# Kernel optimization log

Hardware: AMD Instinct MI355X
Metric: run time of the kernel (lower is better)

The kernel has to match this reference:

```python
import jax, jax.numpy as jnp
import numpy as np
from jax import lax

HEATMAP_THRESH = 0.1


def _conv(x, w, b, stride=1):
    y = lax.conv_general_dilated(x, w, (stride, stride), 'SAME',
                                 dimension_numbers=('NCHW', 'OIHW', 'NCHW'))
    return y + b[None, :, None, None]


def _maxpool2(x):
    return lax.reduce_window(x, -jnp.inf, lax.max, (1, 1, 2, 2), (1, 1, 2, 2), 'VALID')


def _up2(x):
    return jnp.repeat(jnp.repeat(x, 2, axis=2), 2, axis=3)


def _find_peaks_mask(hm, thresh):
    # Vectorized equivalent of the CPU nested-loop _find_peaks:
    # interior pixel is a peak iff v > thresh and v >= its 4 axial neighbors.
    c = hm[:, :, 1:-1, 1:-1]
    m = ((c > thresh)
         & (c >= hm[:, :, :-2, 1:-1]) & (c >= hm[:, :, 2:, 1:-1])
         & (c >= hm[:, :, 1:-1, :-2]) & (c >= hm[:, :, 1:-1, 2:]))
    return jnp.pad(m, ((0, 0), (0, 0), (1, 1), (1, 1)))  # border never a peak


def _param(key, shape):
    fan_in = int(np.prod(shape[1:]))
    return jax.random.normal(key, shape, jnp.float32) / np.sqrt(fan_in)


_SHAPES = {
    'w_d1': (32, 3, 3, 3), 'w_d2': (64, 32, 3, 3), 'w_bn': (128, 64, 3, 3),
    'w_u1': (64, 192, 3, 3), 'w_u2': (32, 96, 3, 3), 'w_seg': (1, 32, 1, 1),
    'w_p1': (64, 4, 3, 3), 'w_p2': (128, 64, 3, 3),
    'w_hm': (17, 128, 1, 1), 'w_paf': (32, 128, 1, 1),
}


def setup_inputs() -> dict:
    key = jax.random.key(0)
    ks = jax.random.split(key, 1 + len(_SHAPES))
    B, H, W = 8, 384, 384
    inp = {'x': jax.random.normal(ks[0], (B, 3, H, W), jnp.float32)}
    for i, (n, s) in enumerate(_SHAPES.items()):
        inp[n] = _param(ks[i + 1], s)
        inp[n.replace('w_', 'b_')] = jnp.zeros((s[0],), jnp.float32)
    return inp


def _forward(x, w_d1, b_d1, w_d2, b_d2, w_bn, b_bn, w_u1, b_u1, w_u2, b_u2,
             w_seg, b_seg, w_p1, b_p1, w_p2, b_p2, w_hm, b_hm, w_paf, b_paf):
    # --- UNet segmentation ---
    d1 = jax.nn.relu(_conv(x, w_d1, b_d1))                    # [B,32,384,384]
    d2 = jax.nn.relu(_conv(_maxpool2(d1), w_d2, b_d2))        # [B,64,192,192]
    bn = jax.nn.relu(_conv(_maxpool2(d2), w_bn, b_bn))        # [B,128,96,96]
    u1 = jax.nn.relu(_conv(jnp.concatenate([_up2(bn), d2], 1), w_u1, b_u1))  # [B,64,192,192]
    u2 = jax.nn.relu(_conv(jnp.concatenate([_up2(u1), d1], 1), w_u2, b_u2))  # [B,32,384,384]
    seg = _conv(u2, w_seg, b_seg)                             # [B,1,384,384]
    # --- Pose net on image + detached seg logits ---
    xp = jnp.concatenate([x, lax.stop_gradient(seg)], axis=1)  # detach()
    p1 = jax.nn.relu(_conv(xp, w_p1, b_p1, stride=2))          # [B,64,192,192]
    p2 = jax.nn.relu(_conv(p1, w_p2, b_p2, stride=2))          # [B,128,96,96]
    hm = _conv(p2, w_hm, b_hm)                                 # [B,17,96,96]
    paf = _conv(p2, w_paf, b_paf)                              # [B,32,96,96]
    return seg, hm, paf


def reference(x, w_d1, b_d1, w_d2, b_d2, w_bn, b_bn, w_u1, b_u1, w_u2, b_u2,
              w_seg, b_seg, w_p1, b_p1, w_p2, b_p2, w_hm, b_hm, w_paf, b_paf):
    seg, hm, paf = _forward(x, w_d1, b_d1, w_d2, b_d2, w_bn, b_bn, w_u1, b_u1,
                            w_u2, b_u2, w_seg, b_seg, w_p1, b_p1, w_p2, b_p2,
                            w_hm, b_hm, w_paf, b_paf)
    # jit-friendly replacement for the variable-length python peak lists:
    # boolean mask over [B,K,h,w]; (x,y) coords recoverable via jnp.nonzero offline.
    peaks = _find_peaks_mask(hm, HEATMAP_THRESH)
    return seg, hm, paf, peaks
```

## Files before the change

### kernel.cpp

```cpp
#include <hip/hip_runtime.h>


#define BS 256
#define BSW 512

typedef _Float16 half8 __attribute__((ext_vector_type(8)));
typedef float floatx4 __attribute__((ext_vector_type(4)));

#define LDSDW 20
#define PLT8 10000
#define ESTR 388

__global__ __launch_bounds__(BS) void packw_gen_kernel(
    const float* __restrict__ w, _Float16* __restrict__ bp, int Cin, int Cout)
{
    int total = (Cin >> 5) * 9 * (Cout >> 4) * 64;
    int tid = blockIdx.x * BS + threadIdx.x;
    if (tid >= total) return;
    int lane = tid & 63;
    int t = tid >> 6;
    int NTl = Cout >> 4;
    int nt = t % NTl; t /= NTl;
    int tap = t % 9;
    int chunk = t / 9;
    int q = lane >> 4, n = lane & 15;
    int co = nt * 16 + n;
    _Float16* ph = bp + (size_t)tid * 8;
    _Float16* pl = bp + (size_t)total * 8 + (size_t)tid * 8;
#pragma unroll
    for (int j = 0; j < 8; ++j) {
        int ci = chunk * 32 + q * 8 + j;
        float v = w[((size_t)co * Cin + ci) * 9 + tap];
        _Float16 h = (_Float16)v;
        ph[j] = h;
        pl[j] = (_Float16)(v - (float)h);
    }
}

__global__ __launch_bounds__(BS) void packw_1x1_kernel(
    const float* __restrict__ w, _Float16* __restrict__ bp, int Cin, int NTl, int Cout)
{
    int total = (Cin >> 5) * NTl * 64;
    int tid = blockIdx.x * BS + threadIdx.x;
    if (tid >= total) return;
    int lane = tid & 63;
    int t = tid >> 6;
    int nt = t % NTl;
    int chunk = t / NTl;
    int q = lane >> 4, n = lane & 15;
    int co = nt * 16 + n;
    _Float16* ph = bp + (size_t)tid * 8;
    _Float16* pl = bp + (size_t)total * 8 + (size_t)tid * 8;
#pragma unroll
    for (int j = 0; j < 8; ++j) {
        int ci = chunk * 32 + q * 8 + j;
        float v = (co < Cout) ? w[(size_t)co * Cin + ci] : 0.f;
        _Float16 h = (_Float16)v;
        ph[j] = h;
        pl[j] = (_Float16)(v - (float)h);
    }
}

__global__ __launch_bounds__(BS) void maxpool2_split_kernel(
    const float* __restrict__ in, _Float16* __restrict__ oh, _Float16* __restrict__ ol,
    int N, int Coct, int H, int W)
{
    int Ho = H >> 1, Wo = W >> 1, Woq = Wo >> 2;
    int idx = blockIdx.x * BS + threadIdx.x;
    int total = N * Coct * Ho * Woq;
    if (idx >= total) return;
    int x4 = idx % Woq;
    int t  = idx / Woq;
    int y  = t % Ho; t /= Ho;
    int oct = t % Coct;
    int n  = t / Coct;
    int C = Coct * 8;
    float m[8][4];
#pragma unroll
    for (int j = 0; j < 8; ++j) {
        const float* r0 = in + ((size_t)((n * C + oct * 8 + j) * H + 2 * y)) * W + 8 * x4;
        const float* r1 = r0 + W;
        float4 a0 = *(const float4*)r0;
        float4 a1 = *(const float4*)(r0 + 4);
        float4 b0 = *(const float4*)r1;
        float4 b1 = *(const float4*)(r1 + 4);
        m[j][0] = fmaxf(fmaxf(a0.x, a0.y), fmaxf(b0.x, b0.y));
        m[j][1] = fmaxf(fmaxf(a0.z, a0.w), fmaxf(b0.z, b0.w));
        m[j][2] = fmaxf(fmaxf(a1.x, a1.y), fmaxf(b1.x, b1.y));
        m[j][3] = fmaxf(fmaxf(a1.z, a1.w), fmaxf(b1.z, b1.w));
    }
#pragma unroll
    for (int p = 0; p < 4; ++p) {
        half8 hv, lv;
#pragma unroll
        for (int j = 0; j < 8; ++j) {
            float v = m[j][p];
            _Float16 h = (_Float16)v;
            hv[j] = h;
            lv[j] = (_Float16)(v - (float)h);
        }
        size_t oa = ((size_t)((n * Coct + oct) * Ho + y) * Wo + 4 * x4 + p) * 8;
        *(half8*)(oh + oa) = hv;
        *(half8*)(ol + oa) = lv;
    }
}

template <int CHUNKS, int NT, int HH, int WW, int OUTMODE>
__global__ __launch_bounds__(BS) void conv3x3s_mfma_kernel(
    const _Float16* __restrict__ inh, const _Float16* __restrict__ inl,
    const _Float16* __restrict__ bp,
    const float* __restrict__ bias,
    float* __restrict__ out,
    _Float16* __restrict__ osph,
    _Float16* __restrict__ ospl)
{
    constexpr int PL = 4 * 34 * LDSDW;
    constexpr int EPI = 64 * NT * 16;
    constexpr int LDS_DW = (2 * PL > EPI) ? 2 * PL : EPI;
    __shared__ unsigned int lds[LDS_DW];

    int xblks = WW / 32;
    int b = blockIdx.x;
    int xb = b % xblks; b /= xblks;
    int yp = b % (HH / 2);
    int n  = b / (HH / 2);
    int y0 = yp * 2;
    int x0 = xb * 32;

    int tid = threadIdx.x;
    int lane = tid & 63, wv = tid >> 6;
    int m = lane & 15, q = lane >> 4;
    int lrow = wv >> 1;
    int lx   = (wv & 1) * 16;

    floatx4 acc[NT];
#pragma unroll
    for (int nt = 0; nt < NT; ++nt) acc[nt] = (floatx4){0.f, 0.f, 0.f, 0.f};

    const int planeW = CHUNKS * 9 * NT * 64 * 8;

    for (int chunk = 0; chunk < CHUNKS; ++chunk) {
        __syncthreads();
        for (int e = tid; e < 4 * 34 * 4; e += BS) {
            int xi = e % 34;
            int rest = e / 34;
            int oct = rest & 3;
            int row = rest >> 2;
            int iy = y0 - 1 + row, gx = x0 - 1 + xi;
            half8 hv = {}, lv = {};
            if (iy >= 0 && iy < HH && gx >= 0 && gx < WW) {
                size_t ga = ((size_t)((n * (CHUNKS * 4) + chunk * 4 + oct) * HH + iy) * WW + gx) * 8;
                hv = *(const half8*)(inh + ga);
                lv = *(const half8*)(inl + ga);
            }
            int base = (row * 34 + xi) * LDSDW + oct * 4;
            *(half8*)((char*)lds + (size_t)base * 4) = hv;
            *(half8*)((char*)lds + ((size_t)PL + base) * 4) = lv;
        }
        __syncthreads();
#pragma unroll
        for (int ky = 0; ky < 3; ++ky) {
#pragma unroll
            for (int kx = 0; kx < 3; ++kx) {
                int row = lrow + ky;
                int xi  = lx + m + kx;
                int adw = (row * 34 + xi) * LDSDW + q * 4;
                half8 ah = *(const half8*)((const char*)lds + (size_t)adw * 4);
                half8 al = *(const half8*)((const char*)lds + ((size_t)PL + adw) * 4);
                int tap = ky * 3 + kx;
                const _Float16* bpp = bp + ((size_t)(chunk * 9 + tap) * NT) * 64 * 8;
#pragma unroll
                for (int nt = 0; nt < NT; ++nt) {
                    half8 bh = *(const half8*)(bpp + ((size_t)nt * 64 + lane) * 8);
                    half8 bl = *(const half8*)(bpp + planeW + ((size_t)nt * 64 + lane) * 8);
                    acc[nt] = __builtin_amdgcn_mfma_f32_16x16x32_f16(ah, bh, acc[nt], 0, 0, 0);
                    acc[nt] = __builtin_amdgcn_mfma_f32_16x16x32_f16(ah, bl, acc[nt], 0, 0, 0);
                    acc[nt] = __builtin_amdgcn_mfma_f32_16x16x32_f16(al, bh, acc[nt], 0, 0, 0);
                }
            }
        }
    }

    __syncthreads();
#pragma unroll
    for (int nt = 0; nt < NT; ++nt) {
#pragma unroll
        for (int r = 0; r < 4; ++r) {
            int co = nt * 16 + m;
            int pxl = wv * 16 + q * 4 + r;
            ((float*)lds)[co * 64 + pxl] = acc[nt][r];
        }
    }
    __syncthreads();
    if (OUTMODE != 1) {
        constexpr int thPerCo = 256 / (NT * 16);
        constexpr int pxPerTh = 64 / thPerCo;
        int co = tid / thPerCo;
        int sub = tid % thPerCo;
        int pxb = sub * pxPerTh;
        float bb = bias[co];
#pragma unroll
        for (int u = 0; u < pxPerTh; u += 4) {
            int p = pxb + u;
            int row = y0 + (p >> 5), xx = x0 + (p & 31);
            const float* lp = (const float*)lds + co * 64 + p;
            float4 vv = *(const float4*)lp;
            vv.x = fmaxf(vv.x + bb, 0.f);
            vv.y = fmaxf(vv.y + bb, 0.f);
            vv.z = fmaxf(vv.z + bb, 0.f);
            vv.w = fmaxf(vv.w + bb, 0.f);
            *(float4*)(out + ((size_t)(n * NT * 16 + co) * HH + row) * WW + xx) = vv;
        }
    }
    if (OUTMODE >= 1) {
        constexpr int OCTS = NT * 2;
        for (int it = tid; it < OCTS * 64; it += BS) {
            int px = it & 63;
            int oct = it >> 6;
            int row = y0 + (px >> 5), xx = x0 + (px & 31);
            half8 hv, lv;
#pragma unroll
            for (int j = 0; j < 8; ++j) {
                float v = fmaxf(((float*)lds)[(oct * 8 + j) * 64 + px] + bias[oct * 8 + j], 0.f);
                _Float16 hh = (_Float16)v;
                hv[j] = hh;
                lv[j] = (_Float16)(v - (float)hh);
            }
            size_t oaddr = ((size_t)((n * OCTS + oct) * HH + row) * WW + xx) * 8;
            *(half8*)(osph + oaddr) = hv;
            *(half8*)(ospl + oaddr) = lv;
        }
    }
}

template <int CHUNKS, int NT, int WI>
__global__ __launch_bounds__(BS) void conv3x3s2s_mfma_kernel(
    const _Float16* __restrict__ inh, const _Float16* __restrict__ inl,
    const _Float16* __restrict__ bp,
    const float* __restrict__ bias,
    _Float16* __restrict__ oh, _Float16* __restrict__ ol_)
{
    constexpr int WO = WI / 2;
    constexpr int PLs = 5 * 68 * LDSDW;
    constexpr int EPI = 64 * NT * 16;
    constexpr int LDS_DW = (2 * PLs > EPI) ? 2 * PLs : EPI;
    __shared__ unsigned int lds[LDS_DW];

    int xblks = WO / 32;
    int b = blockIdx.x;
    int xb = b % xblks; b /= xblks;
    int yp = b % (WO / 2);
    int n  = b / (WO / 2);
    int y0 = yp * 2;
    int x0 = xb * 32;

    int tid = threadIdx.x;
    int lane = tid & 63, wv = tid >> 6;
    int m = lane & 15, q = lane >> 4;
    int lrow = wv >> 1;
    int lx   = (wv & 1) * 16;

    floatx4 acc[NT];
#pragma unroll
    for (int nt = 0; nt < NT; ++nt) acc[nt] = (floatx4){0.f, 0.f, 0.f, 0.f};

    const int planeW = CHUNKS * 9 * NT * 64 * 8;

    for (int chunk = 0; chunk < CHUNKS; ++chunk) {
        __syncthreads();
        for (int e = tid; e < 5 * 68 * 4; e += BS) {
            int xi = e % 68;
            int rest = e / 68;
            int oct = rest & 3;
            int row = rest >> 2;
            int iy = 2 * y0 + row, ix = 2 * x0 + xi;
            half8 hv = {}, lv = {};
            if (xi < 65 && iy < WI && ix < WI) {
                size_t ga = ((size_t)((n * (CHUNKS * 4) + chunk * 4 + oct) * WI + iy) * WI + ix) * 8;
                hv = *(const half8*)(inh + ga);
                lv = *(const half8*)(inl + ga);
            }
            int pos = (xi & 1) * 34 + (xi >> 1);
            int base = (row * 68 + pos) * LDSDW + oct * 4;
            *(half8*)((char*)lds + (size_t)base * 4) = hv;
            *(half8*)((char*)lds + ((size_t)PLs + base) * 4) = lv;
        }
        __syncthreads();
#pragma unroll
        for (int ky = 0; ky < 3; ++ky) {
#pragma unroll
            for (int kx = 0; kx < 3; ++kx) {
                int row = 2 * lrow + ky;
                int pos = (kx & 1) * 34 + (lx + m) + (kx >> 1);
                int adw = (row * 68 + pos) * LDSDW + q * 4;
                half8 ah = *(const half8*)((const char*)lds + (size_t)adw * 4);
                half8 al = *(const half8*)((const char*)lds + ((size_t)PLs + adw) * 4);
                int tap = ky * 3 + kx;
                const _Float16* bpp = bp + ((size_t)(chunk * 9 + tap) * NT) * 64 * 8;
#pragma unroll
                for (int nt = 0; nt < NT; ++nt) {
                    half8 bh = *(const half8*)(bpp + ((size_t)nt * 64 + lane) * 8);
                    half8 bl = *(const half8*)(bpp + planeW + ((size_t)nt * 64 + lane) * 8);
                    acc[nt] = __builtin_amdgcn_mfma_f32_16x16x32_f16(ah, bh, acc[nt], 0, 0, 0);
                    acc[nt] = __builtin_amdgcn_mfma_f32_16x16x32_f16(ah, bl, acc[nt], 0, 0, 0);
                    acc[nt] = __builtin_amdgcn_mfma_f32_16x16x32_f16(al, bh, acc[nt], 0, 0, 0);
                }
            }
        }
    }

    __syncthreads();
#pragma unroll
    for (int nt = 0; nt < NT; ++nt) {
#pragma unroll
        for (int r = 0; r < 4; ++r) {
            int co = nt * 16 + m;
            int pxl = wv * 16 + q * 4 + r;
            ((float*)lds)[co * 64 + pxl] = acc[nt][r];
        }
    }
    __syncthreads();
    {
        constexpr int OCTS = NT * 2;
        for (int it = tid; it < OCTS * 64; it += BS) {
            int px = it & 63;
            int oct = it >> 6;
            int row = y0 + (px >> 5), xx = x0 + (px & 31);
            half8 hv, lv;
#pragma unroll
            for (int j = 0; j < 8; ++j) {
                float v = fmaxf(((float*)lds)[(oct * 8 + j) * 64 + px] + bias[oct * 8 + j], 0.f);
                _Float16 hh = (_Float16)v;
                hv[j] = hh;
                lv[j] = (_Float16)(v - (float)hh);
            }
            size_t oaddr = ((size_t)((n * OCTS + oct) * WO + row) * WO + xx) * 8;
            *(half8*)(oh + oaddr) = hv;
            *(half8*)(ol_ + oaddr) = lv;
        }
    }
}

template <int CHUNKS, int NT>
__global__ __launch_bounds__(BS) void conv1x1s_mfma_kernel(
    const _Float16* __restrict__ inh, const _Float16* __restrict__ inl,
    const _Float16* __restrict__ bp,
    const float* __restrict__ bias,
    float* __restrict__ out,
    int Cout, int HW)
{
    constexpr int PL1 = 64 * LDSDW;
    constexpr int EPI = 64 * NT * 16;
    constexpr int LDS_DW = (2 * PL1 > EPI) ? 2 * PL1 : EPI;
    __shared__ unsigned int lds[LDS_DW];

    int pblks = HW / 64;
    int b = blockIdx.x;
    int pb = b % pblks;
    int n  = b / pblks;
    int sp0 = pb * 64;

    int tid = threadIdx.x;
    int lane = tid & 63, wv = tid >> 6;
    int m = lane & 15, q = lane >> 4;

    floatx4 acc[NT];
#pragma unroll
    for (int nt = 0; nt < NT; ++nt) acc[nt] = (floatx4){0.f, 0.f, 0.f, 0.f};

    const int planeW = CHUNKS * NT * 64 * 8;

    for (int chunk = 0; chunk < CHUNKS; ++chunk) {
        __syncthreads();
        {
            int px = tid & 63;
            int oct = tid >> 6;
            size_t ga = (((size_t)(n * (CHUNKS * 4) + chunk * 4 + oct)) * HW + sp0 + px) * 8;
            half8 hv = *(const half8*)(inh + ga);
            half8 lv = *(const half8*)(inl + ga);
            int base = px * LDSDW + oct * 4;
            *(half8*)((char*)lds + (size_t)base * 4) = hv;
            *(half8*)((char*)lds + ((size_t)PL1 + base) * 4) = lv;
        }
        __syncthreads();
        {
            int adw = (wv * 16 + m) * LDSDW + q * 4;
            half8 ah = *(const half8*)((const char*)lds + (size_t)adw * 4);
            half8 al = *(const half8*)((const char*)lds + ((size_t)PL1 + adw) * 4);
            const _Float16* bpp = bp + ((size_t)chunk * NT) * 64 * 8;
#pragma unroll
            for (int nt = 0; nt < NT; ++nt) {
                half8 bh = *(const half8*)(bpp + ((size_t)nt * 64 + lane) * 8);
                half8 bl = *(const half8*)(bpp + planeW + ((size_t)nt * 64 + lane) * 8);
                acc[nt] = __builtin_amdgcn_mfma_f32_16x16x32_f16(ah, bh, acc[nt], 0, 0, 0);
                acc[nt] = __builtin_amdgcn_mfma_f32_16x16x32_f16(ah, bl, acc[nt], 0, 0, 0);
                acc[nt] = __builtin_amdgcn_mfma_f32_16x16x32_f16(al, bh, acc[nt], 0, 0, 0);
            }
        }
    }

    __syncthreads();
#pragma unroll
    for (int nt = 0; nt < NT; ++nt) {
#pragma unroll
        for (int r = 0; r < 4; ++r) {
            ((float*)lds)[(nt * 16 + m) * 64 + wv * 16 + q * 4 + r] = acc[nt][r];
        }
    }
    __syncthreads();
    {
        constexpr int thPerCo = 256 / (NT * 16);
        constexpr int pxPerTh = 64 / thPerCo;
        int co = tid / thPerCo;
        int g  = tid % thPerCo;
        if (co < Cout) {
            float bb = bias[co];
            const float* lp = (const float*)lds + co * 64 + g * pxPerTh;
            float* op = out + ((size_t)(n * Cout + co)) * HW + sp0 + g * pxPerTh;
#pragma unroll
            for (int u = 0; u < pxPerTh; u += 4) {
                float4 vv = *(const float4*)(lp + u);
                vv.x += bb; vv.y += bb; vv.z += bb; vv.w += bb;
                *(float4*)(op + u) = vv;
            }
        }
    }
}

__global__ __launch_bounds__(BSW) void u1_mfma_kernel(
    const _Float16* __restrict__ bnh, const _Float16* __restrict__ bnl,
    const _Float16* __restrict__ d2h, const _Float16* __restrict__ d2l,
    const _Float16* __restrict__ bp,
    const float* __restrict__ b_u1,
    _Float16* __restrict__ oh, _Float16* __restrict__ ol_)
{
    __shared__ unsigned int lds[2 * PLT8];
    const int Ho = 192, Wo = 192;
    int b = blockIdx.x;
    int xb = b % 4; b /= 4;
    int yb = b % 24;
    int n  = b / 24;
    int y0 = yb * 8;
    int x0 = xb * 48;

    int tid = threadIdx.x;
    int lane = tid & 63, wv = tid >> 6;
    int m = lane & 15, q = lane >> 4;
    int yr = y0 + wv;

    floatx4 acc[3][4];
#pragma unroll
    for (int mt = 0; mt < 3; ++mt)
#pragma unroll
        for (int nt = 0; nt < 4; ++nt) acc[mt][nt] = (floatx4){0.f, 0.f, 0.f, 0.f};

    const int hh0 = (y0 - 1) >> 1;
    const int hx0 = (x0 - 1) >> 1;

    for (int chunk = 0; chunk < 6; ++chunk) {
        __syncthreads();
        if (chunk < 4) {
            for (int e = tid; e < 6 * 26 * 4; e += BSW) {
                int xi = e % 26;
                int rest = e / 26;
                int oct = rest & 3;
                int row = rest >> 2;
                int hy = hh0 + row, hx = hx0 + xi;
                half8 hv = {}, lv = {};
                if (hy >= 0 && hy < 96 && hx >= 0 && hx < 96) {
                    size_t ga = ((size_t)((n * 16 + chunk * 4 + oct) * 96 + hy) * 96 + hx) * 8;
                    hv = *(const half8*)(bnh + ga);
                    lv = *(const half8*)(bnl + ga);
                }
                int base = (row * 50 + xi) * LDSDW + oct * 4;
                *(half8*)((char*)lds + (size_t)base * 4) = hv;
                *(half8*)((char*)lds + ((size_t)PLT8 + base) * 4) = lv;
            }
        } else {
            for (int e = tid; e < 10 * 50 * 4; e += BSW) {
                int xi = e % 50;
                int rest = e / 50;
                int oct = rest & 3;
                int row = rest >> 2;
                int iy = y0 - 1 + row, gx = x0 - 1 + xi;
                half8 hv = {}, lv = {};
                if (iy >= 0 && iy < Ho && gx >= 0 && gx < Wo) {
                    size_t ga = ((size_t)((n * 8 + (chunk - 4) * 4 + oct) * Ho + iy) * Wo + gx) * 8;
                    hv = *(const half8*)(d2h + ga);
                    lv = *(const half8*)(d2l + ga);
                }
                int base = (row * 50 + xi) * LDSDW + oct * 4;
                *(half8*)((char*)lds + (size_t)base * 4) = hv;
                *(half8*)((char*)lds + ((size_t)PLT8 + base) * 4) = lv;
            }
        }
        __syncthreads();
#pragma unroll
        for (int ky = 0; ky < 3; ++ky) {
#pragma unroll
            for (int kx = 0; kx < 3; ++kx) {
                int tap = ky * 3 + kx;
                const _Float16* bpp = bp + ((size_t)(chunk * 9 + tap) * 4) * 64 * 8;
                half8 bh[4], bl[4];
#pragma unroll
                for (int nt = 0; nt < 4; ++nt) {
                    bh[nt] = *(const half8*)(bpp + ((size_t)nt * 64 + lane) * 8);
                    bl[nt] = *(const half8*)(bpp + 110592 + ((size_t)nt * 64 + lane) * 8);
                }
                int row;
                if (chunk < 4) row = ((yr + ky - 1) >> 1) - hh0;
                else           row = wv + ky;
#pragma unroll
                for (int mt = 0; mt < 3; ++mt) {
                    int px = 16 * mt + m;
                    int xi = (chunk < 4) ? (((x0 + px + kx - 1) >> 1) - hx0)
                                         : (px + kx);
                    int adw = (row * 50 + xi) * LDSDW + q * 4;
                    half8 ah = *(const half8*)((const char*)lds + (size_t)adw * 4);
                    half8 al = *(const half8*)((const char*)lds + ((size_t)PLT8 + adw) * 4);
#pragma unroll
                    for (int nt = 0; nt < 4; ++nt) {
                        acc[mt][nt] = __builtin_amdgcn_mfma_f32_16x16x32_f16(ah, bh[nt], acc[mt][nt], 0, 0, 0);
                        acc[mt][nt] = __builtin_amdgcn_mfma_f32_16x16x32_f16(ah, bl[nt], acc[mt][nt], 0, 0, 0);
                        acc[mt][nt] = __builtin_amdgcn_mfma_f32_16x16x32_f16(al, bh[nt], acc[mt][nt], 0, 0, 0);
                    }
                }
            }
        }
    }

#pragma unroll
    for (int h = 0; h < 2; ++h) {
        __syncthreads();
#pragma unroll
        for (int ntl = 0; ntl < 2; ++ntl) {
#pragma unroll
            for (int mt = 0; mt < 3; ++mt) {
#pragma unroll
                for (int r = 0; r < 4; ++r) {
                    ((float*)lds)[(ntl * 16 + m) * ESTR + wv * 48 + 16 * mt + q * 4 + r]
                        = acc[mt][h * 2 + ntl][r];
                }
            }
        }
        __syncthreads();
        for (int it = tid; it < 4 * 384; it += BSW) {
            int px = it % 384;
            int ol = it / 384;
            int row = y0 + px / 48, xx = x0 + px % 48;
            half8 hv, lv;
#pragma unroll
            for (int j = 0; j < 8; ++j) {
                int col = ol * 8 + j;
                float v = fmaxf(((float*)lds)[col * ESTR + px] + b_u1[h * 32 + col], 0.f);
                _Float16 hh = (_Float16)v;
                hv[j] = hh;
                lv[j] = (_Float16)(v - (float)hh);
            }
            size_t oaddr = ((size_t)((n * 8 + h * 4 + ol) * Ho + row) * Wo + xx) * 8;
            *(half8*)(oh + oaddr) = hv;
            *(half8*)(ol_ + oaddr) = lv;
        }
    }
}

__global__ __launch_bounds__(BSW) void u2seg_mfma_kernel(
    const _Float16* __restrict__ u1h, const _Float16* __restrict__ u1l,
    const _Float16* __restrict__ d1h, const _Float16* __restrict__ d1l,
    const _Float16* __restrict__ bp,
    const float* __restrict__ b_u2,
    const float* __restrict__ w_seg,
    const float* __restrict__ b_seg,
    float* __restrict__ seg)
{
    __shared__ unsigned int lds[2 * PLT8];
    const int Ho = 384, Wo = 384;
    int b = blockIdx.x;
    int xb = b % 8; b /= 8;
    int yb = b % 48;
    int n  = b / 48;
    int y0 = yb * 8;
    int x0 = xb * 48;

    int tid = threadIdx.x;
    int lane = tid & 63, wv = tid >> 6;
    int m = lane & 15, q = lane >> 4;
    int yr = y0 + wv;

    floatx4 acc[3][2];
#pragma unroll
    for (int mt = 0; mt < 3; ++mt) {
        acc[mt][0] = (floatx4){0.f, 0.f, 0.f, 0.f};
        acc[mt][1] = (floatx4){0.f, 0.f, 0.f, 0.f};
    }

    const int hh0 = (y0 - 1) >> 1;
    const int hx0 = (x0 - 1) >> 1;

    for (int chunk = 0; chunk < 3; ++chunk) {
        __syncthreads();
        if (chunk < 2) {
            for (int e = tid; e < 6 * 26 * 4; e += BSW) {
                int xi = e % 26;
                int rest = e / 26;
                int oct = rest & 3;
                int row = rest >> 2;
                int hy = hh0 + row, hx = hx0 + xi;
                half8 hv = {}, lv = {};
                if (hy >= 0 && hy < 192 && hx >= 0 && hx < 192) {
                    size_t ga = ((size_t)((n * 8 + chunk * 4 + oct) * 192 + hy) * 192 + hx) * 8;
                    hv = *(const half8*)(u1h + ga);
                    lv = *(const half8*)(u1l + ga);
                }
                int base = (row * 50 + xi) * LDSDW + oct * 4;
                *(half8*)((char*)lds + (size_t)base * 4) = hv;
                *(half8*)((char*)lds + ((size_t)PLT8 + base) * 4) = lv;
            }
        } else {
            for (int e = tid; e < 10 * 50 * 4; e += BSW) {
                int xi = e % 50;
                int rest = e / 50;
                int oct = rest & 3;
                int row = rest >> 2;
                int iy = y0 - 1 + row, gx = x0 - 1 + xi;
                half8 hv = {}, lv = {};
                if (iy >= 0 && iy < Ho && gx >= 0 && gx < Wo) {
                    size_t ga = ((size_t)((n * 4 + oct) * Ho + iy) * Wo + gx) * 8;
                    hv = *(const half8*)(d1h + ga);
                    lv = *(const half8*)(d1l + ga);
                }
                int base = (row * 50 + xi) * LDSDW + oct * 4;
                *(half8*)((char*)lds + (size_t)base * 4) = hv;
                *(half8*)((char*)lds + ((size_t)PLT8 + base) * 4) = lv;
            }
        }
        __syncthreads();
#pragma unroll
        for (int ky = 0; ky < 3; ++ky) {
#pragma unroll
            for (int kx = 0; kx < 3; ++kx) {
                int tap = ky * 3 + kx;
                const _Float16* bpp = bp + ((size_t)(chunk * 9 + tap) * 2) * 64 * 8;
                half8 bh0 = *(const half8*)(bpp + (size_t)lane * 8);
                half8 bl0 = *(const half8*)(bpp + 27648 + (size_t)lane * 8);
                half8 bh1 = *(const half8*)(bpp + ((size_t)64 + lane) * 8);
                half8 bl1 = *(const half8*)(bpp + 27648 + ((size_t)64 + lane) * 8);
                int row;
                if (chunk < 2) row = ((yr + ky - 1) >> 1) - hh0;
                else           row = wv + ky;
#pragma unroll
                for (int mt = 0; mt < 3; ++mt) {
                    int px = 16 * mt + m;
                    int xi = (chunk < 2) ? (((x0 + px + kx - 1) >> 1) - hx0)
                                         : (px + kx);
                    int adw = (row * 50 + xi) * LDSDW + q * 4;
                    half8 ah = *(const half8*)((const char*)lds + (size_t)adw * 4);
                    half8 al = *(const half8*)((const char*)lds + ((size_t)PLT8 + adw) * 4);
                    acc[mt][0] = __builtin_amdgcn_mfma_f32_16x16x32_f16(ah, bh0, acc[mt][0], 0, 0, 0);
                    acc[mt][0] = __builtin_amdgcn_mfma_f32_16x16x32_f16(ah, bl0, acc[mt][0], 0, 0, 0);
                    acc[mt][0] = __builtin_amdgcn_mfma_f32_16x16x32_f16(al, bh0, acc[mt][0], 0, 0, 0);
                    acc[mt][1] = __builtin_amdgcn_mfma_f32_16x16x32_f16(ah, bh1, acc[mt][1], 0, 0, 0);
                    acc[mt][1] = __builtin_amdgcn_mfma_f32_16x16x32_f16(ah, bl1, acc[mt][1], 0, 0, 0);
                    acc[mt][1] = __builtin_amdgcn_mfma_f32_16x16x32_f16(al, bh1, acc[mt][1], 0, 0, 0);
                }
            }
        }
    }

    float bb0 = b_u2[m], bb1 = b_u2[16 + m];
    float ws0 = w_seg[m], ws1 = w_seg[16 + m];
    float bseg = b_seg[0];
#pragma unroll
    for (int mt = 0; mt < 3; ++mt) {
        float sr[4];
#pragma unroll
        for (int r = 0; r < 4; ++r) {
            float p = ws0 * fmaxf(acc[mt][0][r] + bb0, 0.f)
                    + ws1 * fmaxf(acc[mt][1][r] + bb1, 0.f);
            p += __shfl_xor(p, 1);
            p += __shfl_xor(p, 2);
            p += __shfl_xor(p, 4);
            p += __shfl_xor(p, 8);
            sr[r] = p + bseg;
        }
        if (m == 0) {
            float4 o; o.x = sr[0]; o.y = sr[1]; o.z = sr[2]; o.w = sr[3];
            *(float4*)(seg + ((size_t)n * Ho + yr) * Wo + x0 + 16 * mt + q * 4) = o;
        }
    }
}


template <int UPA, int TCO, int SPLIT>
__global__ __launch_bounds__(BS, 2) void conv3x3_x8_kernel(
    const float* __restrict__ inA, int Ca,
    const float* __restrict__ inB, int Cb,
    const float* __restrict__ w, const float* __restrict__ b,
    float* __restrict__ out,
    int N, int H, int W, int Cout, int do_relu,
    _Float16* __restrict__ osph, _Float16* __restrict__ ospl)
{
    const int W8 = W >> 3;
    int idx = blockIdx.x * BS + threadIdx.x;
    int total = N * H * W8;
    if (idx >= total) return;
    int x8 = idx % W8;
    int t  = idx / W8;
    int y  = t % H;
    int n  = t / H;
    int x0 = x8 << 3;
    const int co0 = blockIdx.y * TCO;
    const bool left_ok  = (x0 > 0);
    const bool right_ok = (x0 + 8 < W);
    const int Cin = Ca + Cb;

    float acc[TCO][8];
#pragma unroll
    for (int j = 0; j < TCO; ++j) {
        float bv = b[co0 + j];
#pragma unroll
        for (int p = 0; p < 8; ++p) acc[j][p] = bv;
    }

    for (int ci = 0; ci < Cin; ++ci) {
        float v[3][10];
#pragma unroll
        for (int ky = 0; ky < 3; ++ky) {
            int iy = y + ky - 1;
            if (iy < 0 || iy >= H) {
#pragma unroll
                for (int p = 0; p < 10; ++p) v[ky][p] = 0.f;
                continue;
            }
            if (UPA == 2 && ci < Ca) {
                const float* r = inA + ((size_t)(n * Ca + ci) * (H >> 1) + (iy >> 1)) * (W >> 1);
                int xh = x0 >> 1;
                float sm = left_ok  ? r[xh - 1] : 0.f;
                float4 qq = *(const float4*)(r + xh);
                float s4 = right_ok ? r[xh + 4] : 0.f;
                v[ky][0] = sm;
                v[ky][1] = qq.x; v[ky][2] = qq.x;
                v[ky][3] = qq.y; v[ky][4] = qq.y;
                v[ky][5] = qq.z; v[ky][6] = qq.z;
                v[ky][7] = qq.w; v[ky][8] = qq.w;
                v[ky][9] = s4;
            } else {
                const float* r = (ci < Ca)
                    ? inA + ((size_t)(n * Ca + ci) * H + iy) * W
                    : inB + ((size_t)(n * Cb + (ci - Ca)) * H + iy) * W;
                v[ky][0] = left_ok ? r[x0 - 1] : 0.f;
                float4 q0 = *(const float4*)(r + x0);
                float4 q1 = *(const float4*)(r + x0 + 4);
                v[ky][1] = q0.x; v[ky][2] = q0.y; v[ky][3] = q0.z; v[ky][4] = q0.w;
                v[ky][5] = q1.x; v[ky][6] = q1.y; v[ky][7] = q1.z; v[ky][8] = q1.w;
                v[ky][9] = right_ok ? r[x0 + 8] : 0.f;
            }
        }
#pragma unroll
        for (int j = 0; j < TCO; ++j) {
            const float* wp = w + ((size_t)(co0 + j) * Cin + ci) * 9;
#pragma unroll
            for (int ky = 0; ky < 3; ++ky) {
                float w0 = wp[ky * 3 + 0], w1 = wp[ky * 3 + 1], w2 = wp[ky * 3 + 2];
#pragma unroll
                for (int p = 0; p < 8; ++p)
                    acc[j][p] += w0 * v[ky][p] + w1 * v[ky][p + 1] + w2 * v[ky][p + 2];
            }
        }
    }

    if (SPLIT) {
#pragma unroll
        for (int p = 0; p < 8; ++p) {
            half8 hv, lv;
#pragma unroll
            for (int j = 0; j < 8; ++j) {
                float v = acc[j][p];
                if (do_relu) v = fmaxf(v, 0.f);
                _Float16 hh = (_Float16)v;
                hv[j] = hh;
                lv[j] = (_Float16)(v - (float)hh);
            }
            size_t oaddr = ((size_t)((n * (Cout >> 3) + (co0 >> 3)) * H + y) * W + x0 + p) * 8;
            *(half8*)(osph + oaddr) = hv;
            *(half8*)(ospl + oaddr) = lv;
        }
    } else {
#pragma unroll
        for (int j = 0; j < TCO; ++j) {
#pragma unroll
            for (int p = 0; p < 8; ++p)
                if (do_relu) acc[j][p] = fmaxf(acc[j][p], 0.f);
            float* o = out + ((size_t)(n * Cout + co0 + j) * H + y) * W + x0;
            float4 q0; q0.x = acc[j][0]; q0.y = acc[j][1]; q0.z = acc[j][2]; q0.w = acc[j][3];
            float4 q1; q1.x = acc[j][4]; q1.y = acc[j][5]; q1.z = acc[j][6]; q1.w = acc[j][7];
            *(float4*)o = q0;
            *(float4*)(o + 4) = q1;
        }
    }
}

template <int TCO, int SPLIT>
__global__ __launch_bounds__(BS) void conv3x3_s2_co_kernel(
    const float* __restrict__ inA, int Ca,
    const float* __restrict__ inB, int Cb,
    const float* __restrict__ w, const float* __restrict__ b,
    float* __restrict__ out,
    int N, int Hi, int Wi, int Cout, int do_relu,
    _Float16* __restrict__ osph, _Float16* __restrict__ ospl)
{
    const int Ho = Hi >> 1, Wo = Wi >> 1, Woq = Wo >> 2;
    int idx = blockIdx.x * BS + threadIdx.x;
    int total = N * Ho * Woq;
    if (idx >= total) return;
    int q  = idx % Woq;
    int t  = idx / Woq;
    int oy = t % Ho;
    int n  = t / Ho;
    int ox0 = q << 2;
    int ix0 = ox0 << 1;
    const int co0 = blockIdx.y * TCO;
    const bool right_ok = (ix0 + 8 < Wi);
    const int Cin = Ca + Cb;

    float acc[TCO][4];
#pragma unroll
    for (int j = 0; j < TCO; ++j) {
        float bv = b[co0 + j];
        acc[j][0] = bv; acc[j][1] = bv; acc[j][2] = bv; acc[j][3] = bv;
    }

    for (int ci = 0; ci < Cin; ++ci) {
        const float* base = (ci < Ca)
            ? inA + (size_t)(n * Ca + ci) * Hi * Wi
            : inB + (size_t)(n * Cb + (ci - Ca)) * Hi * Wi;
        float v[3][9];
#pragma unroll
        for (int ky = 0; ky < 3; ++ky) {
            int iy = 2 * oy + ky;
            if (iy >= Hi) {
#pragma unroll
                for (int p = 0; p < 9; ++p) v[ky][p] = 0.f;
                continue;
            }
            const float* r = base + (size_t)iy * Wi + ix0;
            float4 a = *(const float4*)r;
            float4 c = *(const float4*)(r + 4);
            v[ky][0] = a.x; v[ky][1] = a.y; v[ky][2] = a.z; v[ky][3] = a.w;
            v[ky][4] = c.x; v[ky][5] = c.y; v[ky][6] = c.z; v[ky][7] = c.w;
            v[ky][8] = right_ok ? r[8] : 0.f;
        }
#pragma unroll
        for (int j = 0; j < TCO; ++j) {
            const float* wp = w + ((size_t)(co0 + j) * Cin + ci) * 9;
#pragma unroll
            for (int ky = 0; ky < 3; ++ky) {
                float w0 = wp[ky * 3 + 0], w1 = wp[ky * 3 + 1], w2 = wp[ky * 3 + 2];
#pragma unroll
                for (int p = 0; p < 4; ++p)
                    acc[j][p] += w0 * v[ky][2 * p] + w1 * v[ky][2 * p + 1] + w2 * v[ky][2 * p + 2];
            }
        }
    }

    if (SPLIT) {
#pragma unroll
        for (int p = 0; p < 4; ++p) {
            half8 hv, lv;
#pragma unroll
            for (int j = 0; j < 8; ++j) {
                float v = acc[j][p];
                if (do_relu) v = fmaxf(v, 0.f);
                _Float16 hh = (_Float16)v;
                hv[j] = hh;
                lv[j] = (_Float16)(v - (float)hh);
            }
            size_t oaddr = ((size_t)((n * (Cout >> 3) + (co0 >> 3)) * Ho + oy) * Wo + ox0 + p) * 8;
            *(half8*)(osph + oaddr) = hv;
            *(half8*)(ospl + oaddr) = lv;
        }
    } else {
#pragma unroll
        for (int j = 0; j < TCO; ++j) {
            float4 o;
            o.x = acc[j][0]; o.y = acc[j][1]; o.z = acc[j][2]; o.w = acc[j][3];
            if (do_relu) {
                o.x = fmaxf(o.x, 0.f); o.y = fmaxf(o.y, 0.f);
                o.z = fmaxf(o.z, 0.f); o.w = fmaxf(o.w, 0.f);
            }
            *(float4*)(out + ((size_t)(n * Cout + co0 + j) * Ho + oy) * Wo + ox0) = o;
        }
    }
}

__global__ __launch_bounds__(BS) void peaks_kernel(
    const float* __restrict__ hm, float* __restrict__ out,
    int NC, int H, int W, float thresh)
{
    int idx = blockIdx.x * BS + threadIdx.x;
    int total = NC * H * W;
    if (idx >= total) return;
    int x = idx % W;
    int t = idx / W;
    int y = t % H;
    int c = t / H;
    float r = 0.f;
    if (x >= 1 && x < W - 1 && y >= 1 && y < H - 1) {
        const float* base = hm + (size_t)c * H * W;
        float cv = base[y * W + x];
        if (cv > thresh &&
            cv >= base[(y - 1) * W + x] &&
            cv >= base[(y + 1) * W + x] &&
            cv >= base[y * W + (x - 1)] &&
            cv >= base[y * W + (x + 1)])
            r = 1.f;
    }
    out[idx] = r;
}

static inline int nblk(long n) { return (int)((n + BS - 1) / BS); }

extern "C" void kernel_launch(void* const* d_in, const int* in_sizes, int n_in,
                              void* d_out, int out_size, void* d_ws, size_t ws_size,
                              hipStream_t stream)
{
    const float* x     = (const float*)d_in[0];
    const float* w_d1  = (const float*)d_in[1];  const float* b_d1  = (const float*)d_in[2];
    const float* w_d2  = (const float*)d_in[3];  const float* b_d2  = (const float*)d_in[4];
    const float* w_bn  = (const float*)d_in[5];  const float* b_bn  = (const float*)d_in[6];
    const float* w_u1  = (const float*)d_in[7];  const float* b_u1  = (const float*)d_in[8];
    const float* w_u2  = (const float*)d_in[9];  const float* b_u2  = (const float*)d_in[10];
    const float* w_seg = (const float*)d_in[11]; const float* b_seg = (const float*)d_in[12];
    const float* w_p1  = (const float*)d_in[13]; const float* b_p1  = (const float*)d_in[14];
    const float* w_p2  = (const float*)d_in[15]; const float* b_p2  = (const float*)d_in[16];
    const float* w_hm  = (const float*)d_in[17]; const float* b_hm  = (const float*)d_in[18];
    const float* w_paf = (const float*)d_in[19]; const float* b_paf = (const float*)d_in[20];

    const int N = 8, H = 384, W = 384;
    const int H2 = 192, W2 = 192, H4 = 96, W4 = 96;

    float* ws = (float*)d_ws;
    float* d1   = ws + 18874368;
    _Float16* pd1sp_h = (_Float16*)(ws);
    _Float16* pd1sp_l = (_Float16*)(ws + 4718592);
    float* d2f  = ws + 9437184;
    _Float16* d2sp_h = (_Float16*)(ws + 28311552);
    _Float16* d2sp_l = (_Float16*)(ws + 37748736);
    _Float16* pd2sp_h = (_Float16*)(ws + 47185920);
    _Float16* pd2sp_l = (_Float16*)(ws + 49545216);
    _Float16* bnsp_h = (_Float16*)(ws + 18874368);
    _Float16* bnsp_l = (_Float16*)(ws + 23592960);
    _Float16* u1sp_h = (_Float16*)(ws);
    _Float16* u1sp_l = (_Float16*)(ws + 9437184);
    _Float16* d1sp_h = (_Float16*)(ws + 18874368);
    _Float16* d1sp_l = (_Float16*)(ws + 37748736);
    _Float16* p1sp_h = (_Float16*)(ws);
    _Float16* p1sp_l = (_Float16*)(ws + 9437184);
    _Float16* p2sp_h = (_Float16*)(ws + 18874368);
    _Float16* p2sp_l = (_Float16*)(ws + 23592960);

    float* out_seg   = (float*)d_out;
    float* out_hm    = out_seg + 1179648;
    float* out_paf   = out_hm + 1253376;
    float* out_peaks = out_paf + 2359296;
    _Float16* bp_u1  = (_Float16*)(out_seg + 4792320);
    _Float16* bp_u2  = (_Float16*)(out_seg + 4902912);
    _Float16* bp_d2  = (_Float16*)(out_seg + 4930560);
    _Float16* bp_bn  = (_Float16*)(out_seg + 4948992);
    _Float16* bp_p2  = (_Float16*)(out_seg + 5022720);
    _Float16* bp_hm  = (_Float16*)(out_seg + 5096448);
    _Float16* bp_paf = (_Float16*)(out_seg + 5100544);

    packw_gen_kernel<<<nblk(13824), BS, 0, stream>>>(w_u1, bp_u1, 192, 64);
    packw_gen_kernel<<<nblk(3456),  BS, 0, stream>>>(w_u2, bp_u2, 96, 32);
    packw_gen_kernel<<<nblk(2304),  BS, 0, stream>>>(w_d2, bp_d2, 32, 64);
    packw_gen_kernel<<<nblk(9216),  BS, 0, stream>>>(w_bn, bp_bn, 64, 128);
    packw_gen_kernel<<<nblk(9216),  BS, 0, stream>>>(w_p2, bp_p2, 64, 128);
    packw_1x1_kernel<<<nblk(512),   BS, 0, stream>>>(w_hm, bp_hm, 128, 2, 17);
    packw_1x1_kernel<<<nblk(512),   BS, 0, stream>>>(w_paf, bp_paf, 128, 2, 32);
    {
        dim3 g(nblk((long)N * H * (W / 8)), 32 / 8);
        conv3x3_x8_kernel<1, 8, 0><<<g, BS, 0, stream>>>(
            x, 3, nullptr, 0, w_d1, b_d1, d1, N, H, W, 32, 1, nullptr, nullptr);
    }
    maxpool2_split_kernel<<<nblk((long)8 * 4 * 192 * 48), BS, 0, stream>>>(
        d1, pd1sp_h, pd1sp_l, N, 4, H, W);
    conv3x3s_mfma_kernel<1, 4, 192, 192, 2><<<8 * 96 * 6, BS, 0, stream>>>(
        pd1sp_h, pd1sp_l, bp_d2, b_d2, d2f, d2sp_h, d2sp_l);
    maxpool2_split_kernel<<<nblk((long)8 * 8 * 96 * 24), BS, 0, stream>>>(
        d2f, pd2sp_h, pd2sp_l, N, 8, H2, W2);
    conv3x3s_mfma_kernel<2, 8, 96, 96, 1><<<8 * 48 * 3, BS, 0, stream>>>(
        pd2sp_h, pd2sp_l, bp_bn, b_bn, nullptr, bnsp_h, bnsp_l);
    u1_mfma_kernel<<<8 * 24 * 4, BSW, 0, stream>>>(
        bnsp_h, bnsp_l, d2sp_h, d2sp_l, bp_u1, b_u1, u1sp_h, u1sp_l);
    {
        dim3 g(nblk((long)N * H * (W / 8)), 32 / 8);
        conv3x3_x8_kernel<1, 8, 1><<<g, BS, 0, stream>>>(
            x, 3, nullptr, 0, w_d1, b_d1, nullptr, N, H, W, 32, 1, d1sp_h, d1sp_l);
    }
    u2seg_mfma_kernel<<<8 * 48 * 8, BSW, 0, stream>>>(
        u1sp_h, u1sp_l, d1sp_h, d1sp_l, bp_u2, b_u2, w_seg, b_seg, out_seg);
    {
        dim3 g(nblk((long)N * H2 * (W2 / 4)), 64 / 8);
        conv3x3_s2_co_kernel<8, 1><<<g, BS, 0, stream>>>(
            x, 3, out_seg, 1, w_p1, b_p1, nullptr, N, H, W, 64, 1, p1sp_h, p1sp_l);
    }
    conv3x3s2s_mfma_kernel<2, 8, 192><<<8 * 48 * 3, BS, 0, stream>>>(
        p1sp_h, p1sp_l, bp_p2, b_p2, p2sp_h, p2sp_l);
    conv1x1s_mfma_kernel<4, 2><<<8 * 144, BS, 0, stream>>>(
        p2sp_h, p2sp_l, bp_hm, b_hm, out_hm, 17, H4 * W4);
    conv1x1s_mfma_kernel<4, 2><<<8 * 144, BS, 0, stream>>>(
        p2sp_h, p2sp_l, bp_paf, b_paf, out_paf, 32, H4 * W4);
    peaks_kernel<<<nblk((long)N * 17 * H4 * W4), BS, 0, stream>>>(
        out_hm, out_peaks, N * 17, H4, W4, 0.1f);
}
```

Measured before the change: 962.9 us.

## Fuse 2x2 maxpool into d1 and d2 conv epilogues, drop fp32 intermediates

Adds a direct 3x3 conv kernel that computes two d1 rows per thread, applies ReLU, max-pools them, and writes only the pooled hi/lo fp16 split. It also adds an OUTMODE 3 epilogue to the d2 MFMA conv that pools its 2x32 output tile in LDS and writes the pooled split, while still writing d2sp for the skip connection. This removes the full-resolution fp32 d1 and d2 buffers and both standalone maxpool launches, which cuts a large amount of global memory traffic. The cost is a less parallel d1 kernel with more register pressure, and the full d1 is still computed a second time later for the skip path.

```diff
diff --git a/kernel.cpp b/kernel.cpp
--- a/kernel.cpp
+++ b/kernel.cpp
@@ -61,47 +61,97 @@
     }
 }
 
-__global__ __launch_bounds__(BS) void maxpool2_split_kernel(
-    const float* __restrict__ in, _Float16* __restrict__ oh, _Float16* __restrict__ ol,
-    int N, int Coct, int H, int W)
-{
-    int Ho = H >> 1, Wo = W >> 1, Woq = Wo >> 2;
+template <int TCO>
+__global__ __launch_bounds__(BS, 2) void conv3x3_pool_kernel(
+    const float* __restrict__ inA, int Ca,
+    const float* __restrict__ w, const float* __restrict__ b,
+    _Float16* __restrict__ oph, _Float16* __restrict__ opl,
+    int N, int H, int W, int Cout)
+{
+    const int W8 = W >> 3;
+    const int H2 = H >> 1, W2 = W >> 1;
     int idx = blockIdx.x * BS + threadIdx.x;
-    int total = N * Coct * Ho * Woq;
+    int total = N * H2 * W8;
     if (idx >= total) return;
-    int x4 = idx % Woq;
-    int t  = idx / Woq;
-    int y  = t % Ho; t /= Ho;
-    int oct = t % Coct;
-    int n  = t / Coct;
-    int C = Coct * 8;
-    float m[8][4];
-#pragma unroll
-    for (int j = 0; j < 8; ++j) {
-        const float* r0 = in + ((size_t)((n * C + oct * 8 + j) * H + 2 * y)) * W + 8 * x4;
-        const float* r1 = r0 + W;
-        float4 a0 = *(const float4*)r0;
-        float4 a1 = *(const float4*)(r0 + 4);
-        float4 b0 = *(const float4*)r1;
-        float4 b1 = *(const float4*)(r1 + 4);
-        m[j][0] = fmaxf(fmaxf(a0.x, a0.y), fmaxf(b0.x, b0.y));
-        m[j][1] = fmaxf(fmaxf(a0.z, a0.w), fmaxf(b0.z, b0.w));
-        m[j][2] = fmaxf(fmaxf(a1.x, a1.y), fmaxf(b1.x, b1.y));
-        m[j][3] = fmaxf(fmaxf(a1.z, a1.w), fmaxf(b1.z, b1.w));
-    }
-#pragma unroll
-    for (int p = 0; p < 4; ++p) {
+    int x8 = idx % W8;
+    int t  = idx / W8;
+    int yo = t % H2;
+    int n  = t / H2;
+    int x0 = x8 << 3;
+    const int co0 = blockIdx.y * TCO;
+    const bool left_ok  = (x0 > 0);
+    const bool right_ok = (x0 + 8 < W);
+    const int Cin = Ca;
+
+    float pool[TCO][4];
+
+#pragma unroll
+    for (int rr = 0; rr < 2; ++rr) {
+        int y = 2 * yo + rr;
+        float acc[TCO][8];
+#pragma unroll
+        for (int j = 0; j < TCO; ++j) {
+            float bv = b[co0 + j];
+#pragma unroll
+            for (int p = 0; p < 8; ++p) acc[j][p] = bv;
+        }
+
+        for (int ci = 0; ci < Cin; ++ci) {
+            float v[3][10];
+#pragma unroll
+            for (int ky = 0; ky < 3; ++ky) {
+                int iy = y + ky - 1;
+                if (iy < 0 || iy >= H) {
+#pragma unroll
+                    for (int p = 0; p < 10; ++p) v[ky][p] = 0.f;
+                    continue;
+                }
+                const float* r = inA + ((size_t)(n * Ca + ci) * H + iy) * W;
+                v[ky][0] = left_ok ? r[x0 - 1] : 0.f;
+                float4 q0 = *(const float4*)(r + x0);
+                float4 q1 = *(const float4*)(r + x0 + 4);
+                v[ky][1] = q0.x; v[ky][2] = q0.y; v[ky][3] = q0.z; v[ky][4] = q0.w;
+                v[ky][5] = q1.x; v[ky][6] = q1.y; v[ky][7] = q1.z; v[ky][8] = q1.w;
+                v[ky][9] = right_ok ? r[x0 + 8] : 0.f;
+            }
+#pragma unroll
+            for (int j = 0; j < TCO; ++j) {
+                const float* wp = w + ((size_t)(co0 + j) * Cin + ci) * 9;
+#pragma unroll
+                for (int ky = 0; ky < 3; ++ky) {
+                    float w0 = wp[ky * 3 + 0], w1 = wp[ky * 3 + 1], w2 = wp[ky * 3 + 2];
+#pragma unroll
+                    for (int p = 0; p < 8; ++p)
+                        acc[j][p] += w0 * v[ky][p] + w1 * v[ky][p + 1] + w2 * v[ky][p + 2];
+                }
+            }
+        }
+
+#pragma unroll
+        for (int j = 0; j < TCO; ++j) {
+#pragma unroll
+            for (int p4 = 0; p4 < 4; ++p4) {
+                float mrow = fmaxf(fmaxf(acc[j][2 * p4], 0.f),
+                                   fmaxf(acc[j][2 * p4 + 1], 0.f));
+                pool[j][p4] = (rr == 0) ? mrow : fmaxf(pool[j][p4], mrow);
+            }
+        }
+    }
+
+#pragma unroll
+    for (int p4 = 0; p4 < 4; ++p4) {
         half8 hv, lv;
 #pragma unroll
         for (int j = 0; j < 8; ++j) {
-            float v = m[j][p];
-            _Float16 h = (_Float16)v;
-            hv[j] = h;
-            lv[j] = (_Float16)(v - (float)h);
-        }
-        size_t oa = ((size_t)((n * Coct + oct) * Ho + y) * Wo + 4 * x4 + p) * 8;
-        *(half8*)(oh + oa) = hv;
-        *(half8*)(ol + oa) = lv;
+            float v = pool[j][p4];
+            _Float16 hh = (_Float16)v;
+            hv[j] = hh;
+            lv[j] = (_Float16)(v - (float)hh);
+        }
+        size_t oa = ((size_t)((n * (Cout >> 3) + (co0 >> 3)) * H2 + yo) * W2
+                     + (x0 >> 1) + p4) * 8;
+        *(half8*)(oph + oa) = hv;
+        *(half8*)(opl + oa) = lv;
     }
 }
 
@@ -112,7 +162,9 @@
     const float* __restrict__ bias,
     float* __restrict__ out,
     _Float16* __restrict__ osph,
-    _Float16* __restrict__ ospl)
+    _Float16* __restrict__ ospl,
+    _Float16* __restrict__ oph,
+    _Float16* __restrict__ opl)
 {
     constexpr int PL = 4 * 34 * LDSDW;
     constexpr int EPI = 64 * NT * 16;
@@ -192,7 +244,7 @@
         }
     }
     __syncthreads();
-    if (OUTMODE != 1) {
+    if (OUTMODE == 0 || OUTMODE == 2) {
         constexpr int thPerCo = 256 / (NT * 16);
         constexpr int pxPerTh = 64 / thPerCo;
         int co = tid / thPerCo;
@@ -229,6 +281,31 @@
             size_t oaddr = ((size_t)((n * OCTS + oct) * HH + row) * WW + xx) * 8;
             *(half8*)(osph + oaddr) = hv;
             *(half8*)(ospl + oaddr) = lv;
+        }
+    }
+    if (OUTMODE == 3) {
+        constexpr int OCTS = NT * 2;
+        constexpr int HHo = HH / 2, WWo = WW / 2;
+        for (int it = tid; it < OCTS * 16; it += BS) {
+            int xo = it & 15;
+            int oct = it >> 4;
+            half8 hv, lv;
+#pragma unroll
+            for (int j = 0; j < 8; ++j) {
+                const float* base = (const float*)lds + (oct * 8 + j) * 64;
+                float bb = bias[oct * 8 + j];
+                float t0 = fmaxf(fmaxf(base[2 * xo] + bb, 0.f),
+                                 fmaxf(base[2 * xo + 1] + bb, 0.f));
+                float t1 = fmaxf(fmaxf(base[32 + 2 * xo] + bb, 0.f),
+                                 fmaxf(base[32 + 2 * xo + 1] + bb, 0.f));
+                float v = fmaxf(t0, t1);
+                _Float16 hh = (_Float16)v;
+                hv[j] = hh;
+                lv[j] = (_Float16)(v - (float)hh);
+            }
+            size_t oaddr = ((size_t)((n * OCTS + oct) * HHo + yp) * WWo + (x0 >> 1) + xo) * 8;
+            *(half8*)(oph + oaddr) = hv;
+            *(half8*)(opl + oaddr) = lv;
         }
     }
 }
@@ -940,10 +1017,8 @@
     const int H2 = 192, W2 = 192, H4 = 96, W4 = 96;
 
     float* ws = (float*)d_ws;
-    float* d1   = ws + 18874368;
     _Float16* pd1sp_h = (_Float16*)(ws);
     _Float16* pd1sp_l = (_Float16*)(ws + 4718592);
-    float* d2f  = ws + 9437184;
     _Float16* d2sp_h = (_Float16*)(ws + 28311552);
     _Float16* d2sp_l = (_Float16*)(ws + 37748736);
     _Float16* pd2sp_h = (_Float16*)(ws + 47185920);
@@ -979,18 +1054,14 @@
     packw_1x1_kernel<<<nblk(512),   BS, 0, stream>>>(w_hm, bp_hm, 128, 2, 17);
     packw_1x1_kernel<<<nblk(512),   BS, 0, stream>>>(w_paf, bp_paf, 128, 2, 32);
     {
-        dim3 g(nblk((long)N * H * (W / 8)), 32 / 8);
-        conv3x3_x8_kernel<1, 8, 0><<<g, BS, 0, stream>>>(
-            x, 3, nullptr, 0, w_d1, b_d1, d1, N, H, W, 32, 1, nullptr, nullptr);
-    }
-    maxpool2_split_kernel<<<nblk((long)8 * 4 * 192 * 48), BS, 0, stream>>>(
-        d1, pd1sp_h, pd1sp_l, N, 4, H, W);
-    conv3x3s_mfma_kernel<1, 4, 192, 192, 2><<<8 * 96 * 6, BS, 0, stream>>>(
-        pd1sp_h, pd1sp_l, bp_d2, b_d2, d2f, d2sp_h, d2sp_l);
-    maxpool2_split_kernel<<<nblk((long)8 * 8 * 96 * 24), BS, 0, stream>>>(
-        d2f, pd2sp_h, pd2sp_l, N, 8, H2, W2);
+        dim3 g(nblk((long)N * H2 * (W / 8)), 32 / 8);
+        conv3x3_pool_kernel<8><<<g, BS, 0, stream>>>(
+            x, 3, w_d1, b_d1, pd1sp_h, pd1sp_l, N, H, W, 32);
+    }
+    conv3x3s_mfma_kernel<1, 4, 192, 192, 3><<<8 * 96 * 6, BS, 0, stream>>>(
+        pd1sp_h, pd1sp_l, bp_d2, b_d2, nullptr, d2sp_h, d2sp_l, pd2sp_h, pd2sp_l);
     conv3x3s_mfma_kernel<2, 8, 96, 96, 1><<<8 * 48 * 3, BS, 0, stream>>>(
-        pd2sp_h, pd2sp_l, bp_bn, b_bn, nullptr, bnsp_h, bnsp_l);
+        pd2sp_h, pd2sp_l, bp_bn, b_bn, nullptr, bnsp_h, bnsp_l, nullptr, nullptr);
     u1_mfma_kernel<<<8 * 24 * 4, BSW, 0, stream>>>(
         bnsp_h, bnsp_l, d2sp_h, d2sp_l, bp_u1, b_u1, u1sp_h, u1sp_l);
     {
```

Result: faster. 906.5 us (-5.9%).
